# Optimization experiments

Measured on AMD Instinct MI355X. Metric: run time of the kernel, lower is better.

Reference implementation:

```python
import jax, jax.numpy as jnp
import numpy as np

B, D = 4096, 1024

def setup_inputs() -> dict:
    key = jax.random.key(0)
    k1, k2, k3 = jax.random.split(key, 3)
    # q, p are row-stochastic probability distributions (original calls q.log())
    q = jax.nn.softmax(jax.random.normal(k1, (B, D), dtype=jnp.float32), axis=-1)
    p = jax.nn.softmax(jax.random.normal(k2, (B, D), dtype=jnp.float32), axis=-1)
    # binary same-class indicator matrix
    labels_matrix = jax.random.randint(k3, (B, B), 0, 2).astype(jnp.float32)
    return {"q": q, "p": p, "labels_matrix": labels_matrix}

def reference(q, p, labels_matrix):
    d = q.shape[1]
    log_q = jnp.log(q)
    log_p = jnp.log(p)
    # torch kl_div(log_q, p) = p * (log p - log q); mean over feature dim -> [B]
    kl_div = jnp.mean(p * (log_p - log_q), axis=1)
    # pairwise kl_dis[i, j] = mean_d p[j,d] * (log p[j,d] - log q[i,d])
    # = (sum_d p[j] log p[j] - (log_q @ p^T)[i, j]) / D  -- single GEMM, no BxBxD tensor
    p_entropy_term = jnp.sum(p * log_p, axis=1)          # [B]
    cross = log_q @ p.T                                   # [B, B]
    kl_dis = (p_entropy_term[None, :] - cross) / d        # [B, B]
    # original detaches kl_dis via .cpu().numpy()
    kl_dis = jax.lax.stop_gradient(kl_dis)
    positive = kl_div + jnp.sum(kl_dis * labels_matrix, axis=1)
    negative = jnp.sum(kl_dis * (1.0 - labels_matrix), axis=1)
    return jnp.sum(positive / negative)
```

## Files before the change

kernel.cpp:

```cpp
#include <hip/hip_runtime.h>
#include <hip/hip_bf16.h>
#include <stdint.h>

#define BROWS 4096
#define DDIM  1024

typedef __bf16 bf16_t;
typedef __bf16 bf16x8 __attribute__((ext_vector_type(8)));
typedef float  f32x4  __attribute__((ext_vector_type(4)));
typedef unsigned int u32;

#define GEMM_BLOCKS 1024


__device__ __forceinline__ unsigned short f2bf_bits(float f) {
    union { float f; unsigned int u; } v; v.f = f;
    unsigned int u = v.u;
    unsigned int r = (u + 0x7fffu + ((u >> 16) & 1u)) >> 16;
    return (unsigned short)r;
}

__device__ __forceinline__ void gload16(const void* g, void* l) {
    __builtin_amdgcn_global_load_lds(
        (const __attribute__((address_space(1))) u32*)g,
        (__attribute__((address_space(3))) u32*)l, 16, 0, 0);
}

__global__ __launch_bounds__(256) void prep_kernel(
    const float* __restrict__ q, const float* __restrict__ p,
    const float* __restrict__ L,
    bf16_t* __restrict__ lqb, bf16_t* __restrict__ pb,
    uint64_t* __restrict__ Lb,
    float* __restrict__ e, float* __restrict__ kld,
    float* __restrict__ CS, float* __restrict__ CL, float* __restrict__ EL,
    int* __restrict__ done)
{
    const int row = blockIdx.x;
    const int t   = threadIdx.x;
    const int wv  = t >> 6, ln = t & 63;

    const float4* q4 = (const float4*)(q + (size_t)row * DDIM);
    const float4* p4 = (const float4*)(p + (size_t)row * DDIM);
    float4 qv = q4[t];
    float4 pv = p4[t];

    float lq0 = __logf(qv.x), lq1 = __logf(qv.y), lq2 = __logf(qv.z), lq3 = __logf(qv.w);
    float lp0 = __logf(pv.x), lp1 = __logf(pv.y), lp2 = __logf(pv.z), lp3 = __logf(pv.w);

    float esum = pv.x * lp0 + pv.y * lp1 + pv.z * lp2 + pv.w * lp3;
    float ksum = pv.x * (lp0 - lq0) + pv.y * (lp1 - lq1)
               + pv.z * (lp2 - lq2) + pv.w * (lp3 - lq3);

    ushort4 uq, up;
    uq.x = f2bf_bits(lq0); uq.y = f2bf_bits(lq1); uq.z = f2bf_bits(lq2); uq.w = f2bf_bits(lq3);
    up.x = f2bf_bits(pv.x); up.y = f2bf_bits(pv.y); up.z = f2bf_bits(pv.z); up.w = f2bf_bits(pv.w);
    ((ushort4*)(lqb + (size_t)row * DDIM))[t] = uq;
    ((ushort4*)(pb  + (size_t)row * DDIM))[t] = up;

    const float4* L4 = (const float4*)(L + (size_t)row * BROWS);
    #pragma unroll
    for (int s = 0; s < 4; s++) {
        float4 lv = L4[s * 256 + t];
        unsigned long long b0 = __ballot(lv.x != 0.0f);
        unsigned long long b1 = __ballot(lv.y != 0.0f);
        unsigned long long b2 = __ballot(lv.z != 0.0f);
        unsigned long long b3 = __ballot(lv.w != 0.0f);
        if (ln < 4) {
            unsigned long long w = (ln == 0) ? b0 : (ln == 1) ? b1 : (ln == 2) ? b2 : b3;
            Lb[(size_t)row * 64 + (s * 4 + wv) * 4 + ln] = w;
        }
    }

    if (t == 0) { CS[row] = 0.f; CL[row] = 0.f; EL[row] = 0.f; }
    if (row == 0 && t == 0) *done = 0;

    #pragma unroll
    for (int off = 32; off > 0; off >>= 1) {
        esum += __shfl_down(esum, off);
        ksum += __shfl_down(ksum, off);
    }
    __shared__ float se[4], sk[4];
    if (ln == 0) { se[wv] = esum; sk[wv] = ksum; }
    __syncthreads();
    if (t == 0) {
        e[row]   = se[0] + se[1] + se[2] + se[3];
        kld[row] = (sk[0] + sk[1] + sk[2] + sk[3]) * (1.0f / DDIM);
    }
}

__global__ __launch_bounds__(256) void gemm_epi_kernel(
    const bf16_t* __restrict__ Abf,
    const bf16_t* __restrict__ Bbf,
    const uint64_t* __restrict__ Lb,
    const float*  __restrict__ e,
    const float*  __restrict__ kld,
    float* __restrict__ CS, float* __restrict__ CL, float* __restrict__ EL,
    int* __restrict__ done, float* __restrict__ out)
{
    __shared__ __align__(16) bf16_t As[128 * 64];
    __shared__ __align__(16) bf16_t Bs[128 * 64];

    const int t     = threadIdx.x;
    const int b     = blockIdx.x;
    const int xcd   = b & 7;
    const int s     = b >> 3;
    const int i_idx = (xcd >> 2) * 16 + (s >> 3);
    const int j_idx = (xcd & 3) * 8 + (s & 7);
    const int i0    = i_idx * 128;
    const int j0    = j_idx * 128;
    const int wave  = t >> 6;
    const int lane  = t & 63;
    const int q4    = lane >> 4;
    const int ln    = lane & 15;
    const int wrow  = wave & 1;
    const int wcol  = wave >> 1;

    f32x4 acc[4][4];
    #pragma unroll
    for (int a = 0; a < 4; a++)
        #pragma unroll
        for (int bq = 0; bq < 4; bq++)
            acc[a][bq] = (f32x4){0.f, 0.f, 0.f, 0.f};

    const bf16_t* gA[4]; const bf16_t* gB[4];
    char* lA[4]; char* lB[4];
    #pragma unroll
    for (int n = 0; n < 4; n++) {
        const int id   = t + n * 256;
        const int row  = id >> 3;
        const int gcol = ((id & 7) ^ (row & 7)) * 8;
        gA[n] = Abf + (size_t)(i0 + row) * DDIM + gcol;
        gB[n] = Bbf + (size_t)(j0 + row) * DDIM + gcol;
        lA[n] = (char*)As + id * 16;
        lB[n] = (char*)Bs + id * 16;
    }

    const int swz = (ln & 7) << 4;

    #pragma unroll 1
    for (int c = 0; c < DDIM / 64; ++c) {
        __syncthreads();
        #pragma unroll
        for (int n = 0; n < 4; n++) gload16(gA[n] + c * 64, lA[n]);
        #pragma unroll
        for (int n = 0; n < 4; n++) gload16(gB[n] + c * 64, lB[n]);
        __asm__ volatile("s_waitcnt vmcnt(0)" ::: "memory");
        __syncthreads();

        #pragma unroll
        for (int ks = 0; ks < 2; ks++) {
            const int cb = (ks * 64 + q4 * 16) ^ swz;
            bf16x8 af[4], bfr[4];
            #pragma unroll
            for (int mi = 0; mi < 4; mi++)
                af[mi] = *(const bf16x8*)((const char*)As
                           + (wrow * 64 + mi * 16 + ln) * 128 + cb);
            #pragma unroll
            for (int ni = 0; ni < 4; ni++)
                bfr[ni] = *(const bf16x8*)((const char*)Bs
                           + (wcol * 64 + ni * 16 + ln) * 128 + cb);
            #pragma unroll
            for (int mi = 0; mi < 4; mi++)
                #pragma unroll
                for (int ni = 0; ni < 4; ni++)
                    acc[mi][ni] = __builtin_amdgcn_mfma_f32_16x16x32_bf16(
                        af[mi], bfr[ni], acc[mi][ni], 0, 0, 0);
        }
    }

    const int i_base = i0 + wrow * 64;
    const int j_base = j0 + wcol * 64;
    const int wbase  = (j_base >> 8) * 4 + (ln & 3);
    const int bshift = ((j_base & 255) >> 2) + (ln >> 2);

    float e_j[4];
    #pragma unroll
    for (int ni = 0; ni < 4; ni++) e_j[ni] = e[j_base + ni * 16 + ln];

    #pragma unroll
    for (int mi = 0; mi < 4; mi++) {
        #pragma unroll
        for (int r = 0; r < 4; r++) {
            const int i = i_base + mi * 16 + q4 * 4 + r;
            const uint64_t m  = Lb[(size_t)i * 64 + wbase];
            const uint64_t ms = m >> bshift;
            float cs = 0.f, cl = 0.f, el = 0.f;
            #pragma unroll
            for (int ni = 0; ni < 4; ni++) {
                float cv = acc[mi][ni][r];
                cs += cv;
                if ((ms >> (ni * 4)) & 1ull) { cl += cv; el += e_j[ni]; }
            }
            #pragma unroll
            for (int sft = 1; sft < 16; sft <<= 1) {
                cs += __shfl_xor(cs, sft);
                cl += __shfl_xor(cl, sft);
                el += __shfl_xor(el, sft);
            }
            if (ln == 0) {
                atomicAdd(&CS[i], cs);
                atomicAdd(&CL[i], cl);
                atomicAdd(&EL[i], el);
            }
        }
    }

    __asm__ volatile("s_waitcnt vmcnt(0)" ::: "memory");
    __syncthreads();
    __shared__ int sIsLast;
    if (t == 0) sIsLast = (atomicAdd(done, 1) == GEMM_BLOCKS - 1) ? 1 : 0;
    __syncthreads();
    if (sIsLast) {
        __shared__ float sred[4];
        __shared__ float sEtot;
        const int wv = t >> 6;

        float ssum = 0.f;
        #pragma unroll
        for (int j = t; j < BROWS; j += 256) ssum += e[j];
        #pragma unroll
        for (int off = 32; off > 0; off >>= 1) ssum += __shfl_down(ssum, off);
        if (lane == 0) sred[wv] = ssum;
        __syncthreads();
        if (t == 0) {
            float a = 0.f;
            #pragma unroll
            for (int k = 0; k < 4; k++) a += sred[k];
            sEtot = a;
        }
        __syncthreads();
        const float Etot = sEtot;
        const float invD = 1.0f / DDIM;

        float rs = 0.f;
        #pragma unroll
        for (int i = t; i < BROWS; i += 256) {
            float el = __hip_atomic_load(&EL[i], __ATOMIC_RELAXED, __HIP_MEMORY_SCOPE_AGENT);
            float cl = __hip_atomic_load(&CL[i], __ATOMIC_RELAXED, __HIP_MEMORY_SCOPE_AGENT);
            float cs = __hip_atomic_load(&CS[i], __ATOMIC_RELAXED, __HIP_MEMORY_SCOPE_AGENT);
            float pos = kld[i] + (el - cl) * invD;
            float neg = (Etot - el - cs + cl) * invD;
            rs += pos / neg;
        }
        __syncthreads();
        #pragma unroll
        for (int off = 32; off > 0; off >>= 1) rs += __shfl_down(rs, off);
        if (lane == 0) sred[wv] = rs;
        __syncthreads();
        if (t == 0) {
            float a = 0.f;
            #pragma unroll
            for (int k = 0; k < 4; k++) a += sred[k];
            out[0] = a;
        }
    }
}

extern "C" void kernel_launch(void* const* d_in, const int* in_sizes, int n_in,
                              void* d_out, int out_size, void* d_ws, size_t ws_size,
                              hipStream_t stream)
{
    const float* q = (const float*)d_in[0];
    const float* p = (const float*)d_in[1];
    const float* L = (const float*)d_in[2];
    float* out = (float*)d_out;

    char* ws = (char*)d_ws;
    bf16_t* lqb = (bf16_t*)ws;
    bf16_t* pb  = (bf16_t*)(ws + (size_t)BROWS * DDIM * 2);
    float*  e   = (float*)(ws + (size_t)BROWS * DDIM * 4);
    float*  kld = e + BROWS;
    float*  CS  = kld + BROWS;
    float*  CL  = CS + BROWS;
    float*  EL  = CL + BROWS;
    uint64_t* Lb = (uint64_t*)(EL + BROWS);
    int*    done = (int*)(Lb + (size_t)BROWS * 64);

    prep_kernel<<<BROWS, 256, 0, stream>>>(q, p, L, lqb, pb, Lb, e, kld, CS, CL, EL, done);

    gemm_epi_kernel<<<GEMM_BLOCKS, 256, 0, stream>>>(lqb, pb, Lb, e, kld,
                                                     CS, CL, EL, done, out);
}
```

Baseline: 196.9 us.

## Double-buffer LDS tiles to overlap global loads with MFMA compute

The GEMM main loop now uses two LDS buffers per operand. The next K-tile is issued with global_load_lds before the MFMAs on the current tile, so one barrier per iteration replaces two and load latency can hide behind compute. LDS use doubles to 64 KB per block, and launch_bounds now requests 2 blocks per CU, which may constrain registers.

Measured after the change: 195.2 us. No clear change (-0.9%).

```diff
diff --git a/kernel.cpp b/kernel.cpp
--- a/kernel.cpp
+++ b/kernel.cpp
@@ -11,6 +11,7 @@
 typedef unsigned int u32;
 
 #define GEMM_BLOCKS 1024
+#define NKT 16
 
 
 __device__ __forceinline__ unsigned short f2bf_bits(float f) {
@@ -88,7 +89,7 @@
     }
 }
 
-__global__ __launch_bounds__(256) void gemm_epi_kernel(
+__global__ __launch_bounds__(256, 2) void gemm_epi_kernel(
     const bf16_t* __restrict__ Abf,
     const bf16_t* __restrict__ Bbf,
     const uint64_t* __restrict__ Lb,
@@ -97,8 +98,8 @@
     float* __restrict__ CS, float* __restrict__ CL, float* __restrict__ EL,
     int* __restrict__ done, float* __restrict__ out)
 {
-    __shared__ __align__(16) bf16_t As[128 * 64];
-    __shared__ __align__(16) bf16_t Bs[128 * 64];
+    __shared__ __align__(16) bf16_t As[2 * 128 * 64];
+    __shared__ __align__(16) bf16_t Bs[2 * 128 * 64];
 
     const int t     = threadIdx.x;
     const int b     = blockIdx.x;
@@ -110,10 +111,10 @@
     const int j0    = j_idx * 128;
     const int wave  = t >> 6;
     const int lane  = t & 63;
-    const int q4    = lane >> 4;
+    const int q4u   = lane >> 4;
     const int ln    = lane & 15;
-    const int wrow  = wave & 1;
-    const int wcol  = wave >> 1;
+    const int wr    = wave & 1;
+    const int wc    = wave >> 1;
 
     f32x4 acc[4][4];
     #pragma unroll
@@ -122,54 +123,76 @@
         for (int bq = 0; bq < 4; bq++)
             acc[a][bq] = (f32x4){0.f, 0.f, 0.f, 0.f};
 
-    const bf16_t* gA[4]; const bf16_t* gB[4];
-    char* lA[4]; char* lB[4];
+    const bf16_t* gA[4]; const bf16_t* gB[4]; int ld[4];
     #pragma unroll
     for (int n = 0; n < 4; n++) {
-        const int id   = t + n * 256;
-        const int row  = id >> 3;
-        const int gcol = ((id & 7) ^ (row & 7)) * 8;
-        gA[n] = Abf + (size_t)(i0 + row) * DDIM + gcol;
-        gB[n] = Bbf + (size_t)(j0 + row) * DDIM + gcol;
-        lA[n] = (char*)As + id * 16;
-        lB[n] = (char*)Bs + id * 16;
-    }
-
-    const int swz = (ln & 7) << 4;
+        const int id    = t + n * 256;
+        const int row   = id >> 3;
+        const int sslot = (id & 7) ^ (row & 7);
+        gA[n] = Abf + (size_t)(i0 + row) * DDIM + sslot * 8;
+        gB[n] = Bbf + (size_t)(j0 + row) * DDIM + sslot * 8;
+        ld[n] = id * 16;
+    }
+
+    const int arow = (wr * 64 + ln) * 128;
+    const int brow = (wc * 64 + ln) * 128;
+    const int c0   = ((q4u    ) ^ (ln & 7)) * 16;
+    const int c1   = ((4 + q4u) ^ (ln & 7)) * 16;
+
+    #pragma unroll
+    for (int n = 0; n < 4; n++) gload16(gA[n], (char*)As + ld[n]);
+    #pragma unroll
+    for (int n = 0; n < 4; n++) gload16(gB[n], (char*)Bs + ld[n]);
+    __asm__ volatile("s_waitcnt vmcnt(0)" ::: "memory");
+    __builtin_amdgcn_s_barrier();
 
     #pragma unroll 1
-    for (int c = 0; c < DDIM / 64; ++c) {
-        __syncthreads();
-        #pragma unroll
-        for (int n = 0; n < 4; n++) gload16(gA[n] + c * 64, lA[n]);
-        #pragma unroll
-        for (int n = 0; n < 4; n++) gload16(gB[n] + c * 64, lB[n]);
-        __asm__ volatile("s_waitcnt vmcnt(0)" ::: "memory");
-        __syncthreads();
-
-        #pragma unroll
-        for (int ks = 0; ks < 2; ks++) {
-            const int cb = (ks * 64 + q4 * 16) ^ swz;
-            bf16x8 af[4], bfr[4];
-            #pragma unroll
-            for (int mi = 0; mi < 4; mi++)
-                af[mi] = *(const bf16x8*)((const char*)As
-                           + (wrow * 64 + mi * 16 + ln) * 128 + cb);
+    for (int it = 0; it < NKT; ++it) {
+        const int cur = it & 1;
+        const char* Ab = (const char*)As + cur * 16384;
+        const char* Bb = (const char*)Bs + cur * 16384;
+
+        if (it + 1 < NKT) {
+            const int k  = (it + 1) * 64;
+            const int nb = (cur ^ 1) * 16384;
+            #pragma unroll
+            for (int n = 0; n < 4; n++) gload16(gA[n] + k, (char*)As + nb + ld[n]);
+            #pragma unroll
+            for (int n = 0; n < 4; n++) gload16(gB[n] + k, (char*)Bs + nb + ld[n]);
+        }
+
+        bf16x8 a0[4], b0[4], a1[4], b1[4];
+        #pragma unroll
+        for (int f = 0; f < 4; f++) a0[f] = *(const bf16x8*)(Ab + arow + f * 2048 + c0);
+        #pragma unroll
+        for (int f = 0; f < 4; f++) b0[f] = *(const bf16x8*)(Bb + brow + f * 2048 + c0);
+        #pragma unroll
+        for (int f = 0; f < 4; f++) a1[f] = *(const bf16x8*)(Ab + arow + f * 2048 + c1);
+        #pragma unroll
+        for (int f = 0; f < 4; f++) b1[f] = *(const bf16x8*)(Bb + brow + f * 2048 + c1);
+
+        #pragma unroll
+        for (int mi = 0; mi < 4; mi++)
             #pragma unroll
             for (int ni = 0; ni < 4; ni++)
-                bfr[ni] = *(const bf16x8*)((const char*)Bs
-                           + (wcol * 64 + ni * 16 + ln) * 128 + cb);
-            #pragma unroll
-            for (int mi = 0; mi < 4; mi++)
-                #pragma unroll
-                for (int ni = 0; ni < 4; ni++)
-                    acc[mi][ni] = __builtin_amdgcn_mfma_f32_16x16x32_bf16(
-                        af[mi], bfr[ni], acc[mi][ni], 0, 0, 0);
-        }
-    }
-
-    const int i_base = i0 + wrow * 64;
-    const int j_base = j0 + wcol * 64;
+                acc[mi][ni] = __builtin_amdgcn_mfma_f32_16x16x32_bf16(
+                    a0[mi], b0[ni], acc[mi][ni], 0, 0, 0);
+        #pragma unroll
+        for (int mi = 0; mi < 4; mi++)
+            #pragma unroll
+            for (int ni = 0; ni < 4; ni++)
+                acc[mi][ni] = __builtin_amdgcn_mfma_f32_16x16x32_bf16(
+                    a1[mi], b1[ni], acc[mi][ni], 0, 0, 0);
+
+        if (it + 1 < NKT) {
+            __asm__ volatile("s_waitcnt vmcnt(0)" ::: "memory");
+        }
+        __asm__ volatile("" ::: "memory");
+        __builtin_amdgcn_s_barrier();
+    }
+
+    const int i_base = i0 + wr * 64;
+    const int j_base = j0 + wc * 64;
     const int wbase  = (j_base >> 8) * 4 + (ln & 3);
     const int bshift = ((j_base & 255) >> 2) + (ln >> 2);
 
@@ -181,7 +204,7 @@
     for (int mi = 0; mi < 4; mi++) {
         #pragma unroll
         for (int r = 0; r < 4; r++) {
-            const int i = i_base + mi * 16 + q4 * 4 + r;
+            const int i = i_base + mi * 16 + q4u * 4 + r;
             const uint64_t m  = Lb[(size_t)i * 64 + wbase];
             const uint64_t ms = m >> bshift;
             float cs = 0.f, cl = 0.f, el = 0.f;
```
